# Kernel tuning notes

Hardware: AMD Instinct MI355X
Metric: run time of the kernel (lower is better)

Reference implementation:

```python
import jax, jax.numpy as jnp
import numpy as np

N_NODES = 50000
N_REL = 3
N_EDGES = 800000
D_FEAT = 128
D_HID = 128  # == dim_embs so residual + concat dims line up
D_QUERY = 64


def setup_inputs() -> dict:
    key = jax.random.key(0)
    ks = jax.random.split(key, 8)
    s = 1.0 / np.sqrt(D_HID)
    return {
        "x": jax.random.normal(ks[0], (N_NODES, D_FEAT), dtype=jnp.float32),
        "edges": jax.random.randint(ks[1], (N_REL, 2, N_EDGES), 0, N_NODES, dtype=jnp.int64),
        "feat_w": jax.random.normal(ks[2], (D_FEAT, D_HID), dtype=jnp.float32) * s,
        "conv_w": jax.random.normal(ks[3], (2, N_REL, D_HID, D_HID), dtype=jnp.float32) * s,
        "conv_b": jax.random.normal(ks[4], (2, N_REL, D_HID), dtype=jnp.float32) * 0.01,
        "attn_w": jax.random.normal(ks[5], (2, D_HID, D_QUERY), dtype=jnp.float32) * s,
        "attn_q": jax.random.normal(ks[6], (2, D_QUERY), dtype=jnp.float32) * s,
        "concat_w": jax.random.normal(ks[7], (D_HID, 3 * D_HID), dtype=jnp.float32) * s,
    }


def reference(x, edges, feat_w, conv_w, conv_b, attn_w, attn_q, concat_w):
    N = x.shape[0]
    R = edges.shape[0]
    ones_e = jnp.ones((edges.shape[2],), dtype=x.dtype)

    def gconv(h, src, dst, W, b):
        # GraphConv with symmetric ('both') normalization + residual
        deg_out = jnp.clip(jax.ops.segment_sum(ones_e, src, num_segments=N), 1.0)
        deg_in = jnp.clip(jax.ops.segment_sum(ones_e, dst, num_segments=N), 1.0)
        m = (h * jax.lax.rsqrt(deg_out)[:, None]) @ W          # [N, D]
        agg = jax.ops.segment_sum(m[src], dst, num_segments=N)  # gather-scatter [E, D] -> [N, D]
        return agg * jax.lax.rsqrt(deg_in)[:, None] + b + h

    def het_layer(h, l):
        # per-relation conv, then attention-weighted aggregation across relations
        vals = jnp.stack([gconv(h, edges[r, 0], edges[r, 1], conv_w[l, r], conv_b[l, r])
                          for r in range(R)])                   # [R, N, D]
        keys = jnp.tanh(jnp.einsum('rnd,dq->rnq', vals, attn_w[l]))
        scores = jnp.einsum('rnq,q->rn', keys, attn_q[l])       # [R, N]
        attn = jax.nn.softmax(scores, axis=0)                   # softmax over relations
        return jnp.einsum('rn,rnd->nd', attn, vals), attn

    h0 = jnp.tanh(x @ feat_w)            # feature_trans + tanh
    h1, _ = het_layer(h0, 1)             # 1-hop path (convs[1] only)
    t, _ = het_layer(h0, 0)              # 2-hop path: convs[0]
    h2, attn = het_layer(t, 1)           # then convs[1]
    y = jnp.concatenate([h0, h1, h2], axis=-1) @ concat_w.T  # concat_weight (no bias)
    return y, attn.T                      # attn_res: [N, R]
```

## Files before the change

### kernel.cpp

```cpp
#include <hip/hip_runtime.h>

#define NN 50000
#define NE 800000
#define DD 128
#define DQ 64
#define NB 42
#define SL 19048
#define NWW 12500

typedef __attribute__((ext_vector_type(8))) short short8_t;
typedef __attribute__((ext_vector_type(4))) float f32x4;

__device__ __forceinline__ int clampi(int v, int lo, int hi) {
  return v < lo ? lo : (v > hi ? hi : v);
}
__device__ __forceinline__ unsigned short f2bf(float f) {
  unsigned int u = __float_as_uint(f);
  return (unsigned short)((u + 0x7FFFu + ((u >> 16) & 1u)) >> 16);
}
__device__ __forceinline__ float bfl(unsigned int u) { return __uint_as_float(u << 16); }
__device__ __forceinline__ float bfh(unsigned int u) { return __uint_as_float(u & 0xFFFF0000u); }
__device__ __forceinline__ float b2f(short s) {
  return __uint_as_float(((unsigned int)(unsigned short)s) << 16);
}

__global__ __launch_bounds__(512) void hist6_kernel(
    const int* __restrict__ e, unsigned int* __restrict__ hist,
    unsigned char* __restrict__ rank) {
  __shared__ unsigned int lds[NWW];
  const int b = blockIdx.x;
  const int c = blockIdx.y;
  const int r = c >> 1;
  const int a = c & 1;
  const int tid = threadIdx.x;
  for (int i = tid; i < NWW; i += 512) lds[i] = 0u;
  __syncthreads();
  const size_t abase = (size_t)r * 2 * NE + (a ? 0 : NE);
  const int beg = b * SL, end = min(beg + SL, NE);
  if (a == 0) {
    unsigned char* rk = rank + (size_t)r * NE;
    for (int i = beg + tid; i < end; i += 512) {
      int v = clampi(e[abase + i], 0, NN - 1);
      unsigned int sh = (v & 3) * 8;
      unsigned int old = atomicAdd(&lds[v >> 2], 1u << sh);
      rk[i] = (unsigned char)((old >> sh) & 0xFFu);
    }
  } else {
    for (int i = beg + tid; i < end; i += 512) {
      int v = clampi(e[abase + i], 0, NN - 1);
      atomicAdd(&lds[v >> 2], 1u << ((v & 3) * 8));
    }
  }
  __syncthreads();
  unsigned int* outp = hist + ((size_t)c * NB + b) * NWW;
  for (int i = tid; i < NWW; i += 512) outp[i] = lds[i];
}

__global__ __launch_bounds__(256) void sumscan_kernel(
    const unsigned int* __restrict__ hist, int* __restrict__ rowptr,
    int* __restrict__ btot, float* __restrict__ rsqi, float* __restrict__ rsqo) {
  __shared__ int part[256];
  const int g = blockIdx.x;
  const int c = blockIdx.y;
  const int r = c >> 1, a = c & 1;
  const int t = threadIdx.x;
  int cntv[8];
  int s = 0;
  const int w0 = g * 500 + t * 2;
  if (t < 250) {
#pragma unroll
    for (int j = 0; j < 2; ++j) {
      const unsigned int* hp = hist + (size_t)c * NB * NWW + w0 + j;
      unsigned int accA = 0, accB = 0;
#pragma unroll 6
      for (int b = 0; b < NB; ++b) {
        unsigned int v = hp[(size_t)b * NWW];
        accA += v & 0x00FF00FFu;
        accB += (v >> 8) & 0x00FF00FFu;
      }
      int c0 = (int)(accA & 0xFFFFu), c2 = (int)(accA >> 16);
      int c1 = (int)(accB & 0xFFFFu), c3 = (int)(accB >> 16);
      cntv[4 * j + 0] = c0; cntv[4 * j + 1] = c1;
      cntv[4 * j + 2] = c2; cntv[4 * j + 3] = c3;
      int n0 = 4 * (w0 + j);
      float* rq = (a == 0) ? rsqi : rsqo;
      rq[r * NN + n0 + 0] = rsqrtf(fmaxf((float)c0, 1.0f));
      rq[r * NN + n0 + 1] = rsqrtf(fmaxf((float)c1, 1.0f));
      rq[r * NN + n0 + 2] = rsqrtf(fmaxf((float)c2, 1.0f));
      rq[r * NN + n0 + 3] = rsqrtf(fmaxf((float)c3, 1.0f));
      s += c0 + c1 + c2 + c3;
    }
  }
  if (a == 1) return;
  part[t] = s;
  __syncthreads();
  for (int off = 1; off < 256; off <<= 1) {
    int x = (t >= off) ? part[t - off] : 0;
    __syncthreads();
    part[t] += x;
    __syncthreads();
  }
  if (t < 250) {
    int excl = part[t] - s;
    int base = g * 2000 + t * 8;
#pragma unroll
    for (int j = 0; j < 8; ++j) {
      rowptr[r * (NN + 1) + base + j] = excl;
      excl += cntv[j];
    }
  }
  if (t == 255) btot[r * 25 + g] = part[255];
}

__global__ __launch_bounds__(64) void scanp2_kernel(
    const int* __restrict__ btot, int* __restrict__ boff, int* __restrict__ rowptr) {
  if (threadIdx.x == 0) {
    for (int r = 0; r < 3; ++r) {
      int run = 0;
      for (int b = 0; b < 25; ++b) {
        boff[r * 25 + b] = run;
        run += btot[r * 25 + b];
      }
      rowptr[r * (NN + 1) + NN] = run;
    }
  }
}

__global__ __launch_bounds__(256) void bases_kernel(
    const unsigned int* __restrict__ hist, const int* __restrict__ boff,
    int* __restrict__ rowptr, unsigned int* __restrict__ delta32) {
  const int r = blockIdx.y;
  const int g = blockIdx.x;
  const int off = boff[r * 25 + g];
  for (int wl = threadIdx.x; wl < 500; wl += 256) {
    int wi = g * 500 + wl;
    int n0 = 4 * wi;
#pragma unroll
    for (int k = 0; k < 4; ++k) rowptr[r * (NN + 1) + n0 + k] += off;
    const unsigned int* hp = hist + (size_t)(r * 2) * NB * NWW + wi;
    unsigned int run = 0;
#pragma unroll 6
    for (int b = 0; b < NB; ++b) {
      delta32[((size_t)r * NB + b) * NWW + wi] = run;
      run += hp[(size_t)b * NWW];
    }
  }
}

__global__ __launch_bounds__(256) void fillr_kernel(
    const int* __restrict__ e, const unsigned char* __restrict__ rank,
    const unsigned char* __restrict__ delta8, const int* __restrict__ rowptr,
    int* __restrict__ col) {
  const int r = blockIdx.y;
  const int i = blockIdx.x * 256 + threadIdx.x;
  const size_t sbase = (size_t)r * 2 * NE;
  int s = clampi(e[sbase + i], 0, NN - 1);
  int d = clampi(e[sbase + NE + i], 0, NN - 1);
  int b = i / SL;
  int pos = rowptr[r * (NN + 1) + d] +
            (int)delta8[((size_t)r * NB + b) * NN + d] +
            (int)rank[(size_t)r * NE + i];
  pos = clampi(pos, 0, NE - 1);
  col[(size_t)r * NE + pos] = s;
}

__global__ __launch_bounds__(256) void prepw_kernel(
    const float* __restrict__ conv_w, const float* __restrict__ feat_w,
    const float* __restrict__ concat_w, const float* __restrict__ attn_w,
    unsigned short* __restrict__ fw) {
  const int i = blockIdx.x;
  if (i < 10) {
    unsigned short* dst = fw + (size_t)i * 16384;
    for (int e = threadIdx.x; e < 2048; e += 256) {
      int nt = e >> 8, ks = (e >> 6) & 3, lane = e & 63;
      int n = (lane & 15) + nt * 16;
      int kb = (lane >> 4) * 8 + ks * 32;
      unsigned int w[4];
#pragma unroll
      for (int jj = 0; jj < 4; ++jj) {
        int k0 = kb + 2 * jj, k1 = k0 + 1;
        float f0, f1;
        if (i < 6) {
          f0 = conv_w[(size_t)i * 16384 + (size_t)k0 * DD + n];
          f1 = conv_w[(size_t)i * 16384 + (size_t)k1 * DD + n];
        } else if (i == 6) {
          f0 = feat_w[(size_t)k0 * DD + n];
          f1 = feat_w[(size_t)k1 * DD + n];
        } else {
          int p = i - 7;
          f0 = concat_w[(size_t)n * 384 + p * DD + k0];
          f1 = concat_w[(size_t)n * 384 + p * DD + k1];
        }
        w[jj] = (unsigned int)f2bf(f0) | ((unsigned int)f2bf(f1) << 16);
      }
      ((uint4*)dst)[e] = make_uint4(w[0], w[1], w[2], w[3]);
    }
  } else {
    const int l = i - 10;
    unsigned short* dst = fw + (size_t)10 * 16384 + (size_t)l * 8192;
    for (int e = threadIdx.x; e < 1024; e += 256) {
      int nt = e >> 8, ks = (e >> 6) & 3, lane = e & 63;
      int n = (lane & 15) + nt * 16;
      int kb = (lane >> 4) * 8 + ks * 32;
      unsigned int w[4];
#pragma unroll
      for (int jj = 0; jj < 4; ++jj) {
        int k0 = kb + 2 * jj, k1 = k0 + 1;
        float f0 = attn_w[((size_t)l * DD + k0) * DQ + n];
        float f1 = attn_w[((size_t)l * DD + k1) * DQ + n];
        w[jj] = (unsigned int)f2bf(f0) | ((unsigned int)f2bf(f1) << 16);
      }
      ((uint4*)dst)[e] = make_uint4(w[0], w[1], w[2], w[3]);
    }
  }
}

template <int AFP32, int TANH, int EPI, int SIX>
__global__ __launch_bounds__(256) void mgemm_kernel(
    const void* __restrict__ Ap, const unsigned short* __restrict__ fw,
    const float* __restrict__ rsqi, const float* __restrict__ bias,
    const unsigned short* __restrict__ residb, unsigned short* __restrict__ Cb) {
  const size_t ND = (size_t)NN * DD;
  const int rel = blockIdx.y;
  const int wsel = SIX ? (rel + 3) % 6 : rel;
  const int arel = SIX ? rel % 3 : rel;
  const unsigned short* fwp = fw + (size_t)wsel * 16384;
  const float* rsqip = EPI ? rsqi + (size_t)arel * NN : nullptr;
  const float* biasp = EPI ? bias + (size_t)wsel * DD : nullptr;
  unsigned short* Cbp = Cb + (size_t)rel * ND;
  __shared__ unsigned short sF[16384];
  const int tid = threadIdx.x;
  {
    const float4* s = (const float4*)fwp;
    float4* d = (float4*)sF;
#pragma unroll
    for (int i = 0; i < 8; ++i) d[tid + i * 256] = s[tid + i * 256];
  }
  __syncthreads();
  const int w = tid >> 6, l = tid & 63, la = l & 15, gr = l >> 4;
  const int row0 = blockIdx.x * 128 + w * 32;
  if (row0 >= NN) return;
  const bool m1ok = (row0 + 32) <= NN;
  short8_t a[2][4];
#pragma unroll
  for (int m = 0; m < 2; ++m) {
    const int r = row0 + m * 16 + la;
    const bool ok = (m == 0) || m1ok;
    if (AFP32) {
      const float* ap = (const float*)Ap + (size_t)r * DD + gr * 8;
#pragma unroll
      for (int ks = 0; ks < 4; ++ks) {
        short8_t v = (short8_t)0;
        if (ok) {
          float4 x0 = *(const float4*)(ap + ks * 32);
          float4 x1 = *(const float4*)(ap + ks * 32 + 4);
          v[0] = (short)f2bf(x0.x); v[1] = (short)f2bf(x0.y);
          v[2] = (short)f2bf(x0.z); v[3] = (short)f2bf(x0.w);
          v[4] = (short)f2bf(x1.x); v[5] = (short)f2bf(x1.y);
          v[6] = (short)f2bf(x1.z); v[7] = (short)f2bf(x1.w);
        }
        a[m][ks] = v;
      }
    } else {
      const unsigned short* ap =
          (const unsigned short*)Ap + (size_t)arel * ND + (size_t)r * DD + gr * 8;
#pragma unroll
      for (int ks = 0; ks < 4; ++ks)
        a[m][ks] = ok ? *(const short8_t*)(ap + ks * 32) : (short8_t)0;
    }
  }
  f32x4 zero = {0.f, 0.f, 0.f, 0.f};
  f32x4 acc[2][8];
#pragma unroll
  for (int m = 0; m < 2; ++m)
#pragma unroll
    for (int nt = 0; nt < 8; ++nt) acc[m][nt] = zero;
#pragma unroll
  for (int nt = 0; nt < 8; ++nt) {
#pragma unroll
    for (int ks = 0; ks < 4; ++ks) {
      short8_t b = *(const short8_t*)(sF + ((nt * 4 + ks) * 64 + l) * 8);
      acc[0][nt] = __builtin_amdgcn_mfma_f32_16x16x32_bf16(a[0][ks], b, acc[0][nt], 0, 0, 0);
      acc[1][nt] = __builtin_amdgcn_mfma_f32_16x16x32_bf16(a[1][ks], b, acc[1][nt], 0, 0, 0);
    }
  }
#pragma unroll
  for (int m = 0; m < 2; ++m) {
    if (m == 1 && !m1ok) break;
#pragma unroll
    for (int rr = 0; rr < 4; ++rr) {
      const int row = row0 + m * 16 + gr * 4 + rr;
      const float sc = EPI ? rsqip[row] : 0.0f;
#pragma unroll
      for (int nt = 0; nt < 8; ++nt) {
        const int c0 = nt * 16 + la;
        float v = acc[m][nt][rr];
        if (TANH) v = tanhf(v);
        if (EPI) {
          float rv = __uint_as_float((unsigned int)residb[(size_t)row * DD + c0] << 16);
          v = fmaf(v, sc, biasp[c0] + rv);
        }
        Cbp[(size_t)row * DD + c0] = f2bf(v);
      }
    }
  }
}

__global__ __launch_bounds__(512) void mconcat_kernel(
    const unsigned short* __restrict__ h0b, const unsigned short* __restrict__ h1b,
    const unsigned short* __restrict__ h2b, const unsigned short* __restrict__ fwc,
    float* __restrict__ Y) {
  __shared__ unsigned short sF[3 * 16384];
  const int tid = threadIdx.x;
  {
    const float4* s = (const float4*)fwc;
    float4* d = (float4*)sF;
#pragma unroll
    for (int i = 0; i < 12; ++i) d[tid + i * 512] = s[tid + i * 512];
  }
  __syncthreads();
  const int w = tid >> 6, l = tid & 63, la = l & 15, gr = l >> 4;
  const int row0 = blockIdx.x * 256 + w * 32;
  if (row0 >= NN) return;
  const bool m1ok = (row0 + 32) <= NN;
  const unsigned short* hb[3] = {h0b, h1b, h2b};
  f32x4 zero = {0.f, 0.f, 0.f, 0.f};
  f32x4 acc[2][8];
#pragma unroll
  for (int m = 0; m < 2; ++m)
#pragma unroll
    for (int nt = 0; nt < 8; ++nt) acc[m][nt] = zero;
#pragma unroll
  for (int p = 0; p < 3; ++p) {
    short8_t a[2][4];
#pragma unroll
    for (int m = 0; m < 2; ++m) {
      const int r = row0 + m * 16 + la;
      const bool ok = (m == 0) || m1ok;
      const unsigned short* ap = hb[p] + (size_t)r * DD + gr * 8;
#pragma unroll
      for (int ks = 0; ks < 4; ++ks)
        a[m][ks] = ok ? *(const short8_t*)(ap + ks * 32) : (short8_t)0;
    }
    const unsigned short* sfp = sF + p * 16384;
#pragma unroll
    for (int nt = 0; nt < 8; ++nt) {
#pragma unroll
      for (int ks = 0; ks < 4; ++ks) {
        short8_t b = *(const short8_t*)(sfp + ((nt * 4 + ks) * 64 + l) * 8);
        acc[0][nt] = __builtin_amdgcn_mfma_f32_16x16x32_bf16(a[0][ks], b, acc[0][nt], 0, 0, 0);
        acc[1][nt] = __builtin_amdgcn_mfma_f32_16x16x32_bf16(a[1][ks], b, acc[1][nt], 0, 0, 0);
      }
    }
  }
#pragma unroll
  for (int m = 0; m < 2; ++m) {
    if (m == 1 && !m1ok) break;
#pragma unroll
    for (int rr = 0; rr < 4; ++rr) {
      const int row = row0 + m * 16 + gr * 4 + rr;
#pragma unroll
      for (int nt = 0; nt < 8; ++nt)
        Y[(size_t)row * DD + nt * 16 + la] = acc[m][nt][rr];
    }
  }
}

#define ACC8(A, V, C) \
  A[0] = fmaf(bfl((V).x), (C), A[0]); A[1] = fmaf(bfh((V).x), (C), A[1]); \
  A[2] = fmaf(bfl((V).y), (C), A[2]); A[3] = fmaf(bfh((V).y), (C), A[3]); \
  A[4] = fmaf(bfl((V).z), (C), A[4]); A[5] = fmaf(bfh((V).z), (C), A[5]); \
  A[6] = fmaf(bfl((V).w), (C), A[6]); A[7] = fmaf(bfh((V).w), (C), A[7]);

__global__ __launch_bounds__(256) void gatherb_kernel(
    const unsigned short* __restrict__ hb, const int* __restrict__ rowptr,
    const int* __restrict__ col, const float* __restrict__ rsqo,
    unsigned short* __restrict__ ub) {
  const size_t ND = (size_t)NN * DD;
  const int rel = blockIdx.y;
  rowptr += (size_t)rel * (NN + 1);
  col += (size_t)rel * NE;
  rsqo += (size_t)rel * NN;
  ub += (size_t)rel * ND;
  int gid = blockIdx.x * 256 + threadIdx.x;
  int n = gid >> 4;
  int lane = gid & 15;
  int e0 = clampi(rowptr[n], 0, NE);
  int e1 = clampi(rowptr[n + 1], e0, NE);
  const uint4* h4 = (const uint4*)hb;
  float a[8] = {0, 0, 0, 0, 0, 0, 0, 0}, b[8] = {0, 0, 0, 0, 0, 0, 0, 0};
  float c[8] = {0, 0, 0, 0, 0, 0, 0, 0}, d[8] = {0, 0, 0, 0, 0, 0, 0, 0};
  int e = e0;
  for (; e + 7 < e1; e += 8) {
    int s0 = clampi(col[e], 0, NN - 1), s1 = clampi(col[e + 1], 0, NN - 1);
    int s2 = clampi(col[e + 2], 0, NN - 1), s3 = clampi(col[e + 3], 0, NN - 1);
    int s4 = clampi(col[e + 4], 0, NN - 1), s5 = clampi(col[e + 5], 0, NN - 1);
    int s6 = clampi(col[e + 6], 0, NN - 1), s7 = clampi(col[e + 7], 0, NN - 1);
    float c0 = rsqo[s0], c1 = rsqo[s1], c2 = rsqo[s2], c3 = rsqo[s3];
    float c4 = rsqo[s4], c5 = rsqo[s5], c6 = rsqo[s6], c7 = rsqo[s7];
    uint4 v0 = h4[(size_t)s0 * 16 + lane];
    uint4 v1 = h4[(size_t)s1 * 16 + lane];
    uint4 v2 = h4[(size_t)s2 * 16 + lane];
    uint4 v3 = h4[(size_t)s3 * 16 + lane];
    uint4 v4 = h4[(size_t)s4 * 16 + lane];
    uint4 v5 = h4[(size_t)s5 * 16 + lane];
    uint4 v6 = h4[(size_t)s6 * 16 + lane];
    uint4 v7 = h4[(size_t)s7 * 16 + lane];
    ACC8(a, v0, c0) ACC8(b, v1, c1) ACC8(c, v2, c2) ACC8(d, v3, c3)
    ACC8(a, v4, c4) ACC8(b, v5, c5) ACC8(c, v6, c6) ACC8(d, v7, c7)
  }
  for (; e + 3 < e1; e += 4) {
    int s0 = clampi(col[e], 0, NN - 1), s1 = clampi(col[e + 1], 0, NN - 1);
    int s2 = clampi(col[e + 2], 0, NN - 1), s3 = clampi(col[e + 3], 0, NN - 1);
    float c0 = rsqo[s0], c1 = rsqo[s1], c2 = rsqo[s2], c3 = rsqo[s3];
    uint4 v0 = h4[(size_t)s0 * 16 + lane];
    uint4 v1 = h4[(size_t)s1 * 16 + lane];
    uint4 v2 = h4[(size_t)s2 * 16 + lane];
    uint4 v3 = h4[(size_t)s3 * 16 + lane];
    ACC8(a, v0, c0) ACC8(b, v1, c1) ACC8(c, v2, c2) ACC8(d, v3, c3)
  }
  for (; e < e1; ++e) {
    int s0 = clampi(col[e], 0, NN - 1);
    float c0 = rsqo[s0];
    uint4 v0 = h4[(size_t)s0 * 16 + lane];
    ACC8(a, v0, c0)
  }
#pragma unroll
  for (int j = 0; j < 8; ++j) a[j] += b[j] + c[j] + d[j];
  uint4 o;
  o.x = (unsigned int)f2bf(a[0]) | ((unsigned int)f2bf(a[1]) << 16);
  o.y = (unsigned int)f2bf(a[2]) | ((unsigned int)f2bf(a[3]) << 16);
  o.z = (unsigned int)f2bf(a[4]) | ((unsigned int)f2bf(a[5]) << 16);
  o.w = (unsigned int)f2bf(a[6]) | ((unsigned int)f2bf(a[7]) << 16);
  ((uint4*)ub)[gid] = o;
}

template <int TWO>
__global__ __launch_bounds__(256) void mscomb_kernel(
    const unsigned short* __restrict__ Vb, const unsigned short* __restrict__ faB,
    const float* __restrict__ AQB, unsigned short* __restrict__ houtB,
    float* __restrict__ attn_out) {
  const size_t ND = (size_t)NN * DD;
  const int y = TWO ? blockIdx.y : 0;
  const unsigned short* Vp = Vb + (TWO ? (size_t)y * 3 * ND : 0);
  const unsigned short* fa = TWO ? faB + (size_t)(1 - y) * 8192 : faB;
  const float* AQ = TWO ? AQB + (size_t)(1 - y) * DQ : AQB;
  unsigned short* houtb = TWO ? houtB + (size_t)y * ND : houtB;
  __shared__ unsigned short sF[8192];
  __shared__ float sS[4][3][32];
  const int tid = threadIdx.x;
  {
    const float4* s = (const float4*)fa;
    float4* d = (float4*)sF;
#pragma unroll
    for (int i = 0; i < 4; ++i) d[tid + i * 256] = s[tid + i * 256];
  }
  const int w = tid >> 6, l = tid & 63, la = l & 15, gr = l >> 4;
  int row0 = blockIdx.x * 128 + w * 32;
  if (row0 + 32 > NN) row0 = NN - 32;
  short8_t a[3][2][4];
#pragma unroll
  for (int r3 = 0; r3 < 3; ++r3) {
#pragma unroll
    for (int m = 0; m < 2; ++m) {
      const unsigned short* rp =
          Vp + (size_t)r3 * ND + (size_t)(row0 + m * 16 + la) * DD + gr * 8;
#pragma unroll
      for (int ks = 0; ks < 4; ++ks)
        a[r3][m][ks] = *(const short8_t*)(rp + ks * 32);
    }
  }
  __syncthreads();
  float q[4];
#pragma unroll
  for (int nt = 0; nt < 4; ++nt) q[nt] = AQ[la + nt * 16];
#pragma unroll
  for (int r3 = 0; r3 < 3; ++r3) {
    f32x4 zero = {0.f, 0.f, 0.f, 0.f};
    f32x4 acc[2][4];
#pragma unroll
    for (int m = 0; m < 2; ++m)
#pragma unroll
      for (int nt = 0; nt < 4; ++nt) acc[m][nt] = zero;
#pragma unroll
    for (int nt = 0; nt < 4; ++nt) {
#pragma unroll
      for (int ks = 0; ks < 4; ++ks) {
        short8_t b = *(const short8_t*)(sF + ((nt * 4 + ks) * 64 + l) * 8);
        acc[0][nt] = __builtin_amdgcn_mfma_f32_16x16x32_bf16(a[r3][0][ks], b, acc[0][nt], 0, 0, 0);
        acc[1][nt] = __builtin_amdgcn_mfma_f32_16x16x32_bf16(a[r3][1][ks], b, acc[1][nt], 0, 0, 0);
      }
    }
#pragma unroll
    for (int m = 0; m < 2; ++m) {
#pragma unroll
      for (int rr = 0; rr < 4; ++rr) {
        float p = tanhf(acc[m][0][rr]) * q[0] + tanhf(acc[m][1][rr]) * q[1] +
                  tanhf(acc[m][2][rr]) * q[2] + tanhf(acc[m][3][rr]) * q[3];
#pragma unroll
        for (int off = 1; off < 16; off <<= 1) p += __shfl_xor(p, off, 16);
        if (la == 0) sS[w][r3][m * 16 + gr * 4 + rr] = p;
      }
    }
  }
  __syncthreads();
#pragma unroll
  for (int m = 0; m < 2; ++m) {
    const int row = row0 + m * 16 + la;
    float s0 = sS[w][0][m * 16 + la];
    float s1 = sS[w][1][m * 16 + la];
    float s2 = sS[w][2][m * 16 + la];
    float mx = fmaxf(s0, fmaxf(s1, s2));
    float e0 = __expf(s0 - mx), e1 = __expf(s1 - mx), e2 = __expf(s2 - mx);
    float inv = 1.0f / (e0 + e1 + e2);
    float a0 = e0 * inv, a1 = e1 * inv, a2 = e2 * inv;
#pragma unroll
    for (int ks = 0; ks < 4; ++ks) {
      unsigned int ow[4];
#pragma unroll
      for (int jj = 0; jj < 4; ++jj) {
        float v0 = a0 * b2f(a[0][m][ks][2 * jj]) + a1 * b2f(a[1][m][ks][2 * jj]) +
                   a2 * b2f(a[2][m][ks][2 * jj]);
        float v1 = a0 * b2f(a[0][m][ks][2 * jj + 1]) + a1 * b2f(a[1][m][ks][2 * jj + 1]) +
                   a2 * b2f(a[2][m][ks][2 * jj + 1]);
        ow[jj] = (unsigned int)f2bf(v0) | ((unsigned int)f2bf(v1) << 16);
      }
      *(uint4*)(houtb + (size_t)row * DD + gr * 8 + ks * 32) =
          make_uint4(ow[0], ow[1], ow[2], ow[3]);
    }
    if (attn_out != nullptr) {
      attn_out[(size_t)row * 3 + 0] = a0;
      attn_out[(size_t)row * 3 + 1] = a1;
      attn_out[(size_t)row * 3 + 2] = a2;
    }
  }
}

extern "C" void kernel_launch(void* const* d_in, const int* in_sizes, int n_in,
                              void* d_out, int out_size, void* d_ws, size_t ws_size,
                              hipStream_t stream) {
  const float* x        = (const float*)d_in[0];
  const int*   edges    = (const int*)d_in[1];
  const float* feat_w   = (const float*)d_in[2];
  const float* conv_w   = (const float*)d_in[3];
  const float* conv_b   = (const float*)d_in[4];
  const float* attn_w   = (const float*)d_in[5];
  const float* attn_q   = (const float*)d_in[6];
  const float* concat_w = (const float*)d_in[7];
  float* out = (float*)d_out;

  float* ws = (float*)d_ws;
  float* rsqo = ws;
  float* rsqi = rsqo + 3 * NN;
  int* btot = (int*)(rsqi + 3 * NN);
  int* boff = btot + 80;
  int* cnt = boff + 96;
  int* rowptr = cnt + 3 * NN;
  int* col = rowptr + 3 * (NN + 1) + 13;
  const size_t ND = (size_t)NN * DD;
  float* P1 = (float*)(col + 3 * (size_t)NE);
  float* PA = P1 + ND;
  float* PB = PA + ND;
  unsigned short* U0 = (unsigned short*)(PB + ND);
  unsigned short* B0 = U0 + 3 * ND;
  unsigned short* B1 = B0 + ND;
  unsigned short* B2 = B1 + ND;
  unsigned short* fw = (unsigned short*)cnt;
  unsigned int* hist = (unsigned int*)PA;
  unsigned char* delta8 = (unsigned char*)PB;
  unsigned char* rank8 = (unsigned char*)P1;
  unsigned short* VbAll = (unsigned short*)P1;
  unsigned short* fa0 = fw + (size_t)10 * 16384;
  unsigned short* fa1 = fa0 + 8192;

  hist6_kernel<<<dim3(NB, 6), 512, 0, stream>>>(edges, hist, rank8);
  sumscan_kernel<<<dim3(25, 6), 256, 0, stream>>>(hist, rowptr, btot, rsqi, rsqo);
  scanp2_kernel<<<1, 64, 0, stream>>>(btot, boff, rowptr);
  prepw_kernel<<<12, 256, 0, stream>>>(conv_w, feat_w, concat_w, attn_w, fw);
  bases_kernel<<<dim3(25, 3), 256, 0, stream>>>(hist, boff, rowptr, (unsigned int*)delta8);
  fillr_kernel<<<dim3(3125, 3), 256, 0, stream>>>(edges, rank8, delta8, rowptr, col);

  mgemm_kernel<1, 1, 0, 0><<<dim3(391, 1), 256, 0, stream>>>(
      x, fw + (size_t)6 * 16384, nullptr, nullptr, nullptr, B0);

  gatherb_kernel<<<dim3(3125, 3), 256, 0, stream>>>(B0, rowptr, col, rsqo, U0);

  mgemm_kernel<0, 0, 1, 1><<<dim3(391, 6), 256, 0, stream>>>(
      U0, fw, rsqi, conv_b, B0, VbAll);
  mscomb_kernel<1><<<dim3(391, 2), 256, 0, stream>>>(
      VbAll, fa0, attn_q, B1, nullptr);

  gatherb_kernel<<<dim3(3125, 3), 256, 0, stream>>>(B2, rowptr, col, rsqo, U0);
  mgemm_kernel<0, 0, 1, 0><<<dim3(391, 3), 256, 0, stream>>>(
      U0, fw + (size_t)3 * 16384, rsqi, conv_b + (size_t)3 * DD, B2, VbAll);
  mscomb_kernel<0><<<dim3(391, 1), 256, 0, stream>>>(
      VbAll, fa1, attn_q + DQ, U0, out + ND);

  mconcat_kernel<<<196, 512, 0, stream>>>(B0, B1, U0, fw + (size_t)7 * 16384, out);
}
```

Baseline: 427.1 us.

## Merge preprocessing kernels to cut launches and overlap feature GEMM with CSR fill

Weight prep moves into extra blocks of the histogram kernel. The single-thread block-offset scan is folded into bases_kernel, with each block recomputing its own prefix. The feature-transform GEMM with tanh runs as extra blocks inside the CSR fill kernel. This removes three launches and lets independent work share the same grid, at the cost of a 32KB LDS allocation in fill blocks that never use it, which may reduce occupancy for the scatter part.

```diff
diff --git a/kernel.cpp b/kernel.cpp
--- a/kernel.cpp
+++ b/kernel.cpp
@@ -26,13 +26,65 @@
 
 __global__ __launch_bounds__(512) void hist6_kernel(
     const int* __restrict__ e, unsigned int* __restrict__ hist,
-    unsigned char* __restrict__ rank) {
+    unsigned char* __restrict__ rank,
+    const float* __restrict__ conv_w, const float* __restrict__ feat_w,
+    const float* __restrict__ concat_w, const float* __restrict__ attn_w,
+    unsigned short* __restrict__ fw) {
   __shared__ unsigned int lds[NWW];
+  const int c = blockIdx.y;
+  const int tid = threadIdx.x;
+  if (c == 6) {
+    const int i = blockIdx.x;
+    if (i >= 12) return;
+    if (i < 10) {
+      unsigned short* dst = fw + (size_t)i * 16384;
+      for (int eI = tid; eI < 2048; eI += 512) {
+        int nt = eI >> 8, ks = (eI >> 6) & 3, lane = eI & 63;
+        int n = (lane & 15) + nt * 16;
+        int kb = (lane >> 4) * 8 + ks * 32;
+        unsigned int w[4];
+#pragma unroll
+        for (int jj = 0; jj < 4; ++jj) {
+          int k0 = kb + 2 * jj, k1 = k0 + 1;
+          float f0, f1;
+          if (i < 6) {
+            f0 = conv_w[(size_t)i * 16384 + (size_t)k0 * DD + n];
+            f1 = conv_w[(size_t)i * 16384 + (size_t)k1 * DD + n];
+          } else if (i == 6) {
+            f0 = feat_w[(size_t)k0 * DD + n];
+            f1 = feat_w[(size_t)k1 * DD + n];
+          } else {
+            int p = i - 7;
+            f0 = concat_w[(size_t)n * 384 + p * DD + k0];
+            f1 = concat_w[(size_t)n * 384 + p * DD + k1];
+          }
+          w[jj] = (unsigned int)f2bf(f0) | ((unsigned int)f2bf(f1) << 16);
+        }
+        ((uint4*)dst)[eI] = make_uint4(w[0], w[1], w[2], w[3]);
+      }
+    } else {
+      const int l = i - 10;
+      unsigned short* dst = fw + (size_t)10 * 16384 + (size_t)l * 8192;
+      for (int eI = tid; eI < 1024; eI += 512) {
+        int nt = eI >> 8, ks = (eI >> 6) & 3, lane = eI & 63;
+        int n = (lane & 15) + nt * 16;
+        int kb = (lane >> 4) * 8 + ks * 32;
+        unsigned int w[4];
+#pragma unroll
+        for (int jj = 0; jj < 4; ++jj) {
+          int k0 = kb + 2 * jj, k1 = k0 + 1;
+          float f0 = attn_w[((size_t)l * DD + k0) * DQ + n];
+          float f1 = attn_w[((size_t)l * DD + k1) * DQ + n];
+          w[jj] = (unsigned int)f2bf(f0) | ((unsigned int)f2bf(f1) << 16);
+        }
+        ((uint4*)dst)[eI] = make_uint4(w[0], w[1], w[2], w[3]);
+      }
+    }
+    return;
+  }
   const int b = blockIdx.x;
-  const int c = blockIdx.y;
   const int r = c >> 1;
   const int a = c & 1;
-  const int tid = threadIdx.x;
   for (int i = tid; i < NWW; i += 512) lds[i] = 0u;
   __syncthreads();
   const size_t abase = (size_t)r * 2 * NE + (a ? 0 : NE);
@@ -112,105 +164,111 @@
   if (t == 255) btot[r * 25 + g] = part[255];
 }
 
-__global__ __launch_bounds__(64) void scanp2_kernel(
-    const int* __restrict__ btot, int* __restrict__ boff, int* __restrict__ rowptr) {
-  if (threadIdx.x == 0) {
-    for (int r = 0; r < 3; ++r) {
-      int run = 0;
-      for (int b = 0; b < 25; ++b) {
-        boff[r * 25 + b] = run;
-        run += btot[r * 25 + b];
-      }
-      rowptr[r * (NN + 1) + NN] = run;
-    }
-  }
-}
-
 __global__ __launch_bounds__(256) void bases_kernel(
-    const unsigned int* __restrict__ hist, const int* __restrict__ boff,
+    const unsigned int* __restrict__ hist, const int* __restrict__ btot,
     int* __restrict__ rowptr, unsigned int* __restrict__ delta32) {
   const int r = blockIdx.y;
   const int g = blockIdx.x;
-  const int off = boff[r * 25 + g];
+  int run = 0, off = 0;
+#pragma unroll
+  for (int b2 = 0; b2 < 25; ++b2) {
+    if (b2 == g) off = run;
+    run += btot[r * 25 + b2];
+  }
+  if (g == 24 && threadIdx.x == 0) rowptr[r * (NN + 1) + NN] = run;
   for (int wl = threadIdx.x; wl < 500; wl += 256) {
     int wi = g * 500 + wl;
     int n0 = 4 * wi;
 #pragma unroll
     for (int k = 0; k < 4; ++k) rowptr[r * (NN + 1) + n0 + k] += off;
     const unsigned int* hp = hist + (size_t)(r * 2) * NB * NWW + wi;
-    unsigned int run = 0;
+    unsigned int runp = 0;
 #pragma unroll 6
     for (int b = 0; b < NB; ++b) {
-      delta32[((size_t)r * NB + b) * NWW + wi] = run;
-      run += hp[(size_t)b * NWW];
-    }
-  }
-}
-
-__global__ __launch_bounds__(256) void fillr_kernel(
+      delta32[((size_t)r * NB + b) * NWW + wi] = runp;
+      runp += hp[(size_t)b * NWW];
+    }
+  }
+}
+
+__global__ __launch_bounds__(256) void fillfeat_kernel(
     const int* __restrict__ e, const unsigned char* __restrict__ rank,
     const unsigned char* __restrict__ delta8, const int* __restrict__ rowptr,
-    int* __restrict__ col) {
-  const int r = blockIdx.y;
-  const int i = blockIdx.x * 256 + threadIdx.x;
-  const size_t sbase = (size_t)r * 2 * NE;
-  int s = clampi(e[sbase + i], 0, NN - 1);
-  int d = clampi(e[sbase + NE + i], 0, NN - 1);
-  int b = i / SL;
-  int pos = rowptr[r * (NN + 1) + d] +
-            (int)delta8[((size_t)r * NB + b) * NN + d] +
-            (int)rank[(size_t)r * NE + i];
-  pos = clampi(pos, 0, NE - 1);
-  col[(size_t)r * NE + pos] = s;
-}
-
-__global__ __launch_bounds__(256) void prepw_kernel(
-    const float* __restrict__ conv_w, const float* __restrict__ feat_w,
-    const float* __restrict__ concat_w, const float* __restrict__ attn_w,
-    unsigned short* __restrict__ fw) {
-  const int i = blockIdx.x;
-  if (i < 10) {
-    unsigned short* dst = fw + (size_t)i * 16384;
-    for (int e = threadIdx.x; e < 2048; e += 256) {
-      int nt = e >> 8, ks = (e >> 6) & 3, lane = e & 63;
-      int n = (lane & 15) + nt * 16;
-      int kb = (lane >> 4) * 8 + ks * 32;
-      unsigned int w[4];
-#pragma unroll
-      for (int jj = 0; jj < 4; ++jj) {
-        int k0 = kb + 2 * jj, k1 = k0 + 1;
-        float f0, f1;
-        if (i < 6) {
-          f0 = conv_w[(size_t)i * 16384 + (size_t)k0 * DD + n];
-          f1 = conv_w[(size_t)i * 16384 + (size_t)k1 * DD + n];
-        } else if (i == 6) {
-          f0 = feat_w[(size_t)k0 * DD + n];
-          f1 = feat_w[(size_t)k1 * DD + n];
-        } else {
-          int p = i - 7;
-          f0 = concat_w[(size_t)n * 384 + p * DD + k0];
-          f1 = concat_w[(size_t)n * 384 + p * DD + k1];
-        }
-        w[jj] = (unsigned int)f2bf(f0) | ((unsigned int)f2bf(f1) << 16);
-      }
-      ((uint4*)dst)[e] = make_uint4(w[0], w[1], w[2], w[3]);
-    }
-  } else {
-    const int l = i - 10;
-    unsigned short* dst = fw + (size_t)10 * 16384 + (size_t)l * 8192;
-    for (int e = threadIdx.x; e < 1024; e += 256) {
-      int nt = e >> 8, ks = (e >> 6) & 3, lane = e & 63;
-      int n = (lane & 15) + nt * 16;
-      int kb = (lane >> 4) * 8 + ks * 32;
-      unsigned int w[4];
-#pragma unroll
-      for (int jj = 0; jj < 4; ++jj) {
-        int k0 = kb + 2 * jj, k1 = k0 + 1;
-        float f0 = attn_w[((size_t)l * DD + k0) * DQ + n];
-        float f1 = attn_w[((size_t)l * DD + k1) * DQ + n];
-        w[jj] = (unsigned int)f2bf(f0) | ((unsigned int)f2bf(f1) << 16);
-      }
-      ((uint4*)dst)[e] = make_uint4(w[0], w[1], w[2], w[3]);
+    int* __restrict__ col,
+    const float* __restrict__ x, const unsigned short* __restrict__ fwfeat,
+    unsigned short* __restrict__ B0) {
+  __shared__ unsigned short sF[16384];
+  const int tid = threadIdx.x;
+  if (blockIdx.y < 3) {
+    const int r = blockIdx.y;
+    const int i = blockIdx.x * 256 + tid;
+    const size_t sbase = (size_t)r * 2 * NE;
+    int s = clampi(e[sbase + i], 0, NN - 1);
+    int d = clampi(e[sbase + NE + i], 0, NN - 1);
+    int b = i / SL;
+    int pos = rowptr[r * (NN + 1) + d] +
+              (int)delta8[((size_t)r * NB + b) * NN + d] +
+              (int)rank[(size_t)r * NE + i];
+    pos = clampi(pos, 0, NE - 1);
+    col[(size_t)r * NE + pos] = s;
+    return;
+  }
+  if (blockIdx.x >= 391) return;
+  {
+    const float4* s = (const float4*)fwfeat;
+    float4* d = (float4*)sF;
+#pragma unroll
+    for (int i = 0; i < 8; ++i) d[tid + i * 256] = s[tid + i * 256];
+  }
+  __syncthreads();
+  const int w = tid >> 6, l = tid & 63, la = l & 15, gr = l >> 4;
+  const int row0 = blockIdx.x * 128 + w * 32;
+  if (row0 >= NN) return;
+  const bool m1ok = (row0 + 32) <= NN;
+  short8_t a[2][4];
+#pragma unroll
+  for (int m = 0; m < 2; ++m) {
+    const int r = row0 + m * 16 + la;
+    const bool ok = (m == 0) || m1ok;
+    const float* ap = x + (size_t)r * DD + gr * 8;
+#pragma unroll
+    for (int ks = 0; ks < 4; ++ks) {
+      short8_t v = (short8_t)0;
+      if (ok) {
+        float4 x0 = *(const float4*)(ap + ks * 32);
+        float4 x1 = *(const float4*)(ap + ks * 32 + 4);
+        v[0] = (short)f2bf(x0.x); v[1] = (short)f2bf(x0.y);
+        v[2] = (short)f2bf(x0.z); v[3] = (short)f2bf(x0.w);
+        v[4] = (short)f2bf(x1.x); v[5] = (short)f2bf(x1.y);
+        v[6] = (short)f2bf(x1.z); v[7] = (short)f2bf(x1.w);
+      }
+      a[m][ks] = v;
+    }
+  }
+  f32x4 zero = {0.f, 0.f, 0.f, 0.f};
+  f32x4 acc[2][8];
+#pragma unroll
+  for (int m = 0; m < 2; ++m)
+#pragma unroll
+    for (int nt = 0; nt < 8; ++nt) acc[m][nt] = zero;
+#pragma unroll
+  for (int nt = 0; nt < 8; ++nt) {
+#pragma unroll
+    for (int ks = 0; ks < 4; ++ks) {
+      short8_t b = *(const short8_t*)(sF + ((nt * 4 + ks) * 64 + l) * 8);
+      acc[0][nt] = __builtin_amdgcn_mfma_f32_16x16x32_bf16(a[0][ks], b, acc[0][nt], 0, 0, 0);
+      acc[1][nt] = __builtin_amdgcn_mfma_f32_16x16x32_bf16(a[1][ks], b, acc[1][nt], 0, 0, 0);
+    }
+  }
+#pragma unroll
+  for (int m = 0; m < 2; ++m) {
+    if (m == 1 && !m1ok) break;
+#pragma unroll
+    for (int rr = 0; rr < 4; ++rr) {
+      const int row = row0 + m * 16 + gr * 4 + rr;
+#pragma unroll
+      for (int nt = 0; nt < 8; ++nt)
+        B0[(size_t)row * DD + nt * 16 + la] = f2bf(tanhf(acc[m][nt][rr]));
     }
   }
 }
@@ -573,15 +631,12 @@
   unsigned short* fa0 = fw + (size_t)10 * 16384;
   unsigned short* fa1 = fa0 + 8192;
 
-  hist6_kernel<<<dim3(NB, 6), 512, 0, stream>>>(edges, hist, rank8);
+  hist6_kernel<<<dim3(NB, 7), 512, 0, stream>>>(
+      edges, hist, rank8, conv_w, feat_w, concat_w, attn_w, fw);
   sumscan_kernel<<<dim3(25, 6), 256, 0, stream>>>(hist, rowptr, btot, rsqi, rsqo);
-  scanp2_kernel<<<1, 64, 0, stream>>>(btot, boff, rowptr);
-  prepw_kernel<<<12, 256, 0, stream>>>(conv_w, feat_w, concat_w, attn_w, fw);
-  bases_kernel<<<dim3(25, 3), 256, 0, stream>>>(hist, boff, rowptr, (unsigned int*)delta8);
-  fillr_kernel<<<dim3(3125, 3), 256, 0, stream>>>(edges, rank8, delta8, rowptr, col);
-
-  mgemm_kernel<1, 1, 0, 0><<<dim3(391, 1), 256, 0, stream>>>(
-      x, fw + (size_t)6 * 16384, nullptr, nullptr, nullptr, B0);
+  bases_kernel<<<dim3(25, 3), 256, 0, stream>>>(hist, btot, rowptr, (unsigned int*)delta8);
+  fillfeat_kernel<<<dim3(3125, 4), 256, 0, stream>>>(
+      edges, rank8, delta8, rowptr, col, x, fw + (size_t)6 * 16384, B0);
 
   gatherb_kernel<<<dim3(3125, 3), 256, 0, stream>>>(B0, rowptr, col, rsqo, U0);
 
```

Measured after the change: 422.2 us. Within noise of the previous version (-1.2%).
